# Kernel tuning notes

Measured on AMD Instinct MI355X. Metric: run time of the kernel, lower is better.

The kernel has to match this reference:

```python
import jax, jax.numpy as jnp
import numpy as np

P = 16
IMG_SIZES = [(512, 512), (512, 384), (448, 512), (384, 384), (320, 448), (256, 512), (384, 256), (512, 320)]
LMAX = 1024
B, DIM, HEADS, DH, DEPTH, MLP, NC = 8, 512, 8, 64, 6, 2048, 1000
PD = 3 * P * P  # 768 patch dim


def layer_norm(x, w, b=None, eps=1e-5):
    mu = x.mean(-1, keepdims=True)
    var = ((x - mu) ** 2).mean(-1, keepdims=True)
    y = (x - mu) * jax.lax.rsqrt(var + eps) * w
    return y + b if b is not None else y


def _pack(images):
    # slice each image to its true (static) resolution, patchify, pad to LMAX
    toks, his, wis, msks = [], [], [], []
    for i, (H, W) in enumerate(IMG_SIZES):
        h, w = H // P, W // P
        L = h * w
        img = images[i, :, :H, :W]
        t = img.reshape(3, h, P, w, P).transpose(1, 3, 0, 2, 4).reshape(L, PD)
        hi = jnp.repeat(jnp.arange(h), w)
        wi = jnp.tile(jnp.arange(w), h)
        pad = LMAX - L
        toks.append(jnp.pad(t, ((0, pad), (0, 0))))
        his.append(jnp.pad(hi, (0, pad)))
        wis.append(jnp.pad(wi, (0, pad)))
        msks.append(jnp.arange(LMAX) < L)
    return jnp.stack(toks), jnp.stack(his), jnp.stack(wis), jnp.stack(msks)


def _mha(qx, kx, kmask, wq, wk, wv, qn, kn, wo):
    Bq, Lq, _ = qx.shape
    Lk = kx.shape[1]
    q = (qx @ wq.T).reshape(Bq, Lq, HEADS, DH)
    k = (kx @ wk.T).reshape(Bq, Lk, HEADS, DH)
    v = (kx @ wv.T).reshape(Bq, Lk, HEADS, DH)
    q = layer_norm(q, qn)
    k = layer_norm(k, kn)
    s = jnp.einsum('bqhd,bkhd->bhqk', q, k) / np.sqrt(DH).astype(np.float32)
    s = s + jnp.where(kmask[:, None, None, :], 0.0, -1e9)
    a = jax.nn.softmax(s, axis=-1)
    o = jnp.einsum('bhqk,bkhd->bqhd', a, v).reshape(Bq, Lq, HEADS * DH)
    return o @ wo.T


def setup_inputs() -> dict:
    key = jax.random.key(0)
    ks = iter(jax.random.split(key, 48))

    def nrm(shape, s=0.02):
        return jax.random.normal(next(ks), shape, jnp.float32) * s

    return {
        'images': jax.random.normal(next(ks), (B, 3, 512, 512), jnp.float32),
        'pe_ln1_w': jnp.ones(PD), 'pe_ln1_b': jnp.zeros(PD),
        'pe_w': nrm((DIM, PD)), 'pe_b': jnp.zeros(DIM),
        'pe_ln2_w': jnp.ones(DIM), 'pe_ln2_b': jnp.zeros(DIM),
        'pos_h': nrm((32, DIM), 1.0), 'pos_w': nrm((32, DIM), 1.0),
        'attn_ln': jnp.ones((DEPTH, DIM)),
        'wq': nrm((DEPTH, DIM, DIM)), 'wk': nrm((DEPTH, DIM, DIM)), 'wv': nrm((DEPTH, DIM, DIM)),
        'qn': jnp.ones((DEPTH, DH)), 'kn': jnp.ones((DEPTH, DH)),
        'wo': nrm((DEPTH, DIM, DIM)),
        'ff_ln': jnp.ones((DEPTH, DIM)),
        'ff_w1': nrm((DEPTH, MLP, DIM)), 'ff_b1': jnp.zeros((DEPTH, MLP)),
        'ff_w2': nrm((DEPTH, DIM, MLP)), 'ff_b2': jnp.zeros((DEPTH, DIM)),
        'final_ln': jnp.ones(DIM),
        'pool_q': nrm((DIM,), 1.0), 'pool_ln': jnp.ones(DIM),
        'pool_wq': nrm((DIM, DIM)), 'pool_wk': nrm((DIM, DIM)), 'pool_wv': nrm((DIM, DIM)),
        'pool_qn': jnp.ones(DH), 'pool_kn': jnp.ones(DH),
        'pool_wo': nrm((DIM, DIM)),
        'head_ln': jnp.ones(DIM), 'head_w': nrm((NC, DIM)),
    }


def reference(images, pe_ln1_w, pe_ln1_b, pe_w, pe_b, pe_ln2_w, pe_ln2_b, pos_h, pos_w,
              attn_ln, wq, wk, wv, qn, kn, wo, ff_ln, ff_w1, ff_b1, ff_w2, ff_b2,
              final_ln, pool_q, pool_ln, pool_wq, pool_wk, pool_wv, pool_qn, pool_kn,
              pool_wo, head_ln, head_w):
    tok, hi, wi, mask = _pack(images)
    t = layer_norm(tok, pe_ln1_w, pe_ln1_b)
    t = t @ pe_w.T + pe_b
    t = layer_norm(t, pe_ln2_w, pe_ln2_b)
    t = t + pos_h[hi] + pos_w[wi]
    t = t * mask[..., None]
    for l in range(DEPTH):
        xn = layer_norm(t, attn_ln[l])
        t = t + _mha(xn, xn, mask, wq[l], wk[l], wv[l], qn[l], kn[l], wo[l])
        h = layer_norm(t, ff_ln[l])
        t = t + (jax.nn.gelu(h @ ff_w1[l].T + ff_b1[l], approximate=False) @ ff_w2[l].T + ff_b2[l])
    t = layer_norm(t, final_ln)
    # attention pooling: one learned query per image; context = transformer output (unnormed inside attn)
    q = jnp.broadcast_to(pool_q, (B, 1, DIM))
    qn_ = layer_norm(q, pool_ln)
    pooled = _mha(qn_, t, mask, pool_wq, pool_wk, pool_wv, pool_qn, pool_kn, pool_wo)[:, 0]
    return layer_norm(pooled, head_ln) @ head_w.T
```

## Files before the change

kernel.cpp:

```cpp
#include <hip/hip_runtime.h>
#include <math.h>

#define LMAXS 1024
#define NB 8
#define DIM 512
#define HEADS 8
#define DH 64
#define DEPTH 6
#define MLP 2048
#define NC 1000
#define PDIM 768
#define MPACK 5376
#define MVALID 5360

typedef __attribute__((ext_vector_type(8))) short short8;
typedef __attribute__((ext_vector_type(4))) float floatx4;
typedef unsigned short ushort;

__constant__ int c_w[8]   = {32,24,32,24,28,32,16,20};
__constant__ int c_L[8]   = {1024,768,896,576,560,512,384,640};
__constant__ int c_off[9] = {0,1024,1792,2688,3264,3824,4336,4720,5360};

__device__ __forceinline__ int row2img(int r) {
  int b = 0;
  #pragma unroll
  for (int i = 1; i < 8; ++i) if (r >= c_off[i]) b = i;
  return b;
}

__device__ __forceinline__ ushort f2bf(float x) {
  unsigned int u = __float_as_uint(x);
  u += 0x7fff + ((u >> 16) & 1);
  return (ushort)(u >> 16);
}

#define GLOAD_LDS16(gp, lp) \
  __builtin_amdgcn_global_load_lds((const __attribute__((address_space(1))) void*)(gp), \
                                   (__attribute__((address_space(3))) void*)(lp), 16, 0, 0)

__device__ __forceinline__ void reduce2_256(float& s, float& s2, float* red) {
  #pragma unroll
  for (int off = 32; off; off >>= 1) {
    s  += __shfl_xor(s, off);
    s2 += __shfl_xor(s2, off);
  }
  int wv = threadIdx.x >> 6;
  if ((threadIdx.x & 63) == 0) { red[wv*2] = s; red[wv*2+1] = s2; }
  __syncthreads();
  s  = red[0] + red[2] + red[4] + red[6];
  s2 = red[1] + red[3] + red[5] + red[7];
  __syncthreads();
}

__global__ __launch_bounds__(256) void cvt_k(const float* __restrict__ s, ushort* __restrict__ d, int n) {
  int i = blockIdx.x*256 + threadIdx.x;
  if (i < n) d[i] = f2bf(s[i]);
}
__global__ __launch_bounds__(256) void cvt_qkv_k(
    const float* __restrict__ wq, const float* __restrict__ wk, const float* __restrict__ wv,
    ushort* __restrict__ d) {
  int i = blockIdx.x*256 + threadIdx.x;
  if (i >= 6*1536*512) return;
  int l = i / (1536*512), r = (i / 512) % 1536, k = i & 511;
  const float* src = (r < 512) ? wq : (r < 1024) ? wk : wv;
  int rr = r & 511;
  d[i] = f2bf(src[(size_t)l*DIM*DIM + (size_t)rr*DIM + k]);
}
__global__ __launch_bounds__(256) void cvt_pool_k(
    const float* __restrict__ wk, const float* __restrict__ wv, ushort* __restrict__ d) {
  int i = blockIdx.x*256 + threadIdx.x;
  if (i >= 1024*512) return;
  int r = i >> 9, k = i & 511;
  d[i] = f2bf(r < 512 ? wk[(size_t)r*DIM + k] : wv[(size_t)(r-512)*DIM + k]);
}

__global__ __launch_bounds__(256) void pack_ln1_k(
    const float* __restrict__ images, const float* __restrict__ g,
    const float* __restrict__ bb, ushort* __restrict__ tok) {
  int r = blockIdx.x;
  ushort* out = tok + (size_t)r * PDIM;
  if (r >= MVALID) {
    for (int i = threadIdx.x; i < PDIM; i += 256) out[i] = 0;
    return;
  }
  int b = row2img(r), l = r - c_off[b];
  int wgrid = c_w[b];
  __shared__ float vals[PDIM];
  __shared__ float red[8];
  int hp = l / wgrid, wp = l % wgrid;
  const float* base = images + (size_t)b*3*512*512 + (size_t)hp*16*512 + wp*16;
  float s = 0.f, s2 = 0.f;
  for (int i = threadIdx.x; i < PDIM; i += 256) {
    int c = i >> 8, rr = (i >> 4) & 15, cc = i & 15;
    float v = base[(size_t)c*512*512 + rr*512 + cc];
    vals[i] = v; s += v; s2 += v*v;
  }
  reduce2_256(s, s2, red);
  float mu = s * (1.f/PDIM);
  float rs = rsqrtf(fmaxf(s2*(1.f/PDIM) - mu*mu, 0.f) + 1e-5f);
  for (int i = threadIdx.x; i < PDIM; i += 256)
    out[i] = f2bf((vals[i]-mu)*rs*g[i] + bb[i]);
}

template<int ACT, int OUT>
__global__ __launch_bounds__(256) void gemm_bf(
    const ushort* __restrict__ A, const ushort* __restrict__ W,
    const float* __restrict__ bias, void* __restrict__ Cv,
    int M, int N, int K) {
  __shared__ ushort As[128*64];
  __shared__ ushort Ws[128*64];
  int tid = threadIdx.x;
  int row0 = blockIdx.y*128, col0 = blockIdx.x*128;
  int lane = tid & 63, l15 = lane & 15, quad = lane >> 4;
  int wv = tid >> 6, wm = wv >> 1, wn = wv & 1;
  int sw = l15 & 7;
  int segA = (quad ^ sw) * 8, segB = segA ^ 32;
  const ushort *Ap[4], *Wp[4];
  #pragma unroll
  for (int j = 0; j < 4; ++j) {
    int blk = j*256 + tid;
    int r = blk >> 3, s = ((blk & 7) ^ (r & 7)) * 8;
    Ap[j] = A + (size_t)(row0 + r)*K + s;
    Wp[j] = W + (size_t)(col0 + r)*K + s;
  }
  int ksl = K / gridDim.z;
  int kb0 = blockIdx.z * ksl;
  floatx4 acc[4][4] = {};
  for (int k0 = kb0; k0 < kb0 + ksl; k0 += 64) {
    __syncthreads();
    #pragma unroll
    for (int j = 0; j < 4; ++j) {
      GLOAD_LDS16(Ap[j] + k0, &As[(j*256+tid)*8]);
      GLOAD_LDS16(Wp[j] + k0, &Ws[(j*256+tid)*8]);
    }
    __syncthreads();
    #pragma unroll
    for (int w = 0; w < 2; ++w) {
      int sg = w ? segB : segA;
      short8 af[4], bf[4];
      #pragma unroll
      for (int i = 0; i < 4; ++i) af[i] = *(const short8*)&As[(wm*64 + i*16 + l15)*64 + sg];
      #pragma unroll
      for (int j = 0; j < 4; ++j) bf[j] = *(const short8*)&Ws[(wn*64 + j*16 + l15)*64 + sg];
      #pragma unroll
      for (int i = 0; i < 4; ++i)
        #pragma unroll
        for (int j = 0; j < 4; ++j)
          acc[i][j] = __builtin_amdgcn_mfma_f32_16x16x32_bf16(af[i], bf[j], acc[i][j], 0, 0, 0);
    }
  }
  int rb = row0 + wm*64 + quad*4;
  int cb = col0 + wn*64 + l15;
  bool addb = (bias != nullptr) && (blockIdx.z == 0);
  #pragma unroll
  for (int j = 0; j < 4; ++j) {
    int cc = cb + j*16;
    float bsum = addb ? bias[cc] : 0.f;
    #pragma unroll
    for (int i = 0; i < 4; ++i) {
      int rr = rb + i*16;
      #pragma unroll
      for (int reg = 0; reg < 4; ++reg) {
        float v = acc[i][j][reg] + bsum;
        if (ACT == 1) v = 0.5f*v*(1.f + erff(v*0.70710678118654752f));
        size_t idx = (size_t)(rr + reg)*N + cc;
        if (OUT == 0)      ((float*)Cv)[idx] = v;
        else if (OUT == 1) unsafeAtomicAdd(&((float*)Cv)[idx], v);
        else               ((ushort*)Cv)[idx] = f2bf(v);
      }
    }
  }
}

template<int POOL>
__global__ __launch_bounds__(256) void gemm_qkv_k(
    const ushort* __restrict__ A, const ushort* __restrict__ W,
    const float* __restrict__ gq, const float* __restrict__ gk,
    ushort* __restrict__ Qh, ushort* __restrict__ Kh, ushort* __restrict__ Vh,
    float* __restrict__ KV, int N) {
  const int K = DIM;
  __shared__ ushort As[128*64];
  __shared__ ushort Ws[128*64];
  int tid = threadIdx.x;
  int row0 = blockIdx.y*128, col0 = blockIdx.x*128;
  int lane = tid & 63, l15 = lane & 15, quad = lane >> 4;
  int wv = tid >> 6, wm = wv >> 1, wn = wv & 1;
  int sw = l15 & 7;
  int segA = (quad ^ sw) * 8, segB = segA ^ 32;
  const ushort *Ap[4], *Wp[4];
  #pragma unroll
  for (int j = 0; j < 4; ++j) {
    int blk = j*256 + tid;
    int r = blk >> 3, s = ((blk & 7) ^ (r & 7)) * 8;
    Ap[j] = A + (size_t)(row0 + r)*K + s;
    Wp[j] = W + (size_t)(col0 + r)*K + s;
  }
  floatx4 acc[4][4] = {};
  for (int k0 = 0; k0 < K; k0 += 64) {
    __syncthreads();
    #pragma unroll
    for (int j = 0; j < 4; ++j) {
      GLOAD_LDS16(Ap[j] + k0, &As[(j*256+tid)*8]);
      GLOAD_LDS16(Wp[j] + k0, &Ws[(j*256+tid)*8]);
    }
    __syncthreads();
    #pragma unroll
    for (int w = 0; w < 2; ++w) {
      int sg = w ? segB : segA;
      short8 af[4], bf[4];
      #pragma unroll
      for (int i = 0; i < 4; ++i) af[i] = *(const short8*)&As[(wm*64 + i*16 + l15)*64 + sg];
      #pragma unroll
      for (int j = 0; j < 4; ++j) bf[j] = *(const short8*)&Ws[(wn*64 + j*16 + l15)*64 + sg];
      #pragma unroll
      for (int i = 0; i < 4; ++i)
        #pragma unroll
        for (int j = 0; j < 4; ++j)
          acc[i][j] = __builtin_amdgcn_mfma_f32_16x16x32_bf16(af[i], bf[j], acc[i][j], 0, 0, 0);
    }
  }
  int unit = (col0 >> 6) + wn;
  bool needln = POOL ? (unit < 8) : (unit < 16);
  const float* gain = POOL ? gq : (unit < 8 ? gq : gk);
  #pragma unroll
  for (int i = 0; i < 4; ++i) {
    float s[4] = {0,0,0,0}, s2[4] = {0,0,0,0};
    if (needln) {
      #pragma unroll
      for (int j = 0; j < 4; ++j)
        #pragma unroll
        for (int reg = 0; reg < 4; ++reg) {
          float v = acc[i][j][reg];
          s[reg] += v; s2[reg] += v*v;
        }
      #pragma unroll
      for (int reg = 0; reg < 4; ++reg)
        #pragma unroll
        for (int off = 1; off < 16; off <<= 1) {
          s[reg]  += __shfl_xor(s[reg],  off);
          s2[reg] += __shfl_xor(s2[reg], off);
        }
    }
    #pragma unroll
    for (int reg = 0; reg < 4; ++reg) {
      int r = row0 + wm*64 + i*16 + quad*4 + reg;
      if (r >= MVALID) continue;
      float mu = s[reg]*(1.f/64.f);
      float rs = rsqrtf(fmaxf(s2[reg]*(1.f/64.f) - mu*mu, 0.f) + 1e-5f);
      int b = row2img(r), l = r - c_off[b];
      #pragma unroll
      for (int j = 0; j < 4; ++j) {
        int dh = j*16 + l15;
        float v = acc[i][j][reg];
        if (needln) v = (v - mu)*rs*gain[dh];
        if (POOL) {
          KV[(size_t)r*1024 + unit*64 + dh] = v;
        } else {
          int h = unit & 7;
          size_t dst = ((size_t)(b*8+h)*LMAXS + l)*64 + dh;
          if (unit < 8)       Qh[dst] = f2bf(v);
          else if (unit < 16) Kh[dst] = f2bf(v);
          else                Vh[dst] = f2bf(v);
        }
      }
    }
  }
}

__global__ __launch_bounds__(256) void row_ln_bf_k(
    const float* __restrict__ X, const float* __restrict__ g,
    ushort* __restrict__ Y, int n) {
  __shared__ float red[8];
  size_t base = (size_t)blockIdx.x * n;
  float s=0.f, s2=0.f;
  for (int i = threadIdx.x; i < n; i += 256) { float v = X[base+i]; s += v; s2 += v*v; }
  reduce2_256(s, s2, red);
  float mu = s/n, rs = rsqrtf(fmaxf(s2/n - mu*mu, 0.f) + 1e-5f);
  for (int i = threadIdx.x; i < n; i += 256)
    Y[base+i] = f2bf((X[base+i]-mu)*rs*g[i]);
}

__global__ __launch_bounds__(256) void ln2_pos_k(
    float* __restrict__ T, const float* __restrict__ g, const float* __restrict__ bb,
    const float* __restrict__ ph, const float* __restrict__ pw) {
  int r = blockIdx.x;
  float* x = T + (size_t)r * DIM;
  if (r >= MVALID) {
    for (int i = threadIdx.x; i < DIM; i += 256) x[i] = 0.f;
    return;
  }
  int b = row2img(r), l = r - c_off[b];
  __shared__ float red[8];
  int wgrid = c_w[b];
  int hi = l / wgrid, wi = l % wgrid;
  float s=0.f, s2=0.f;
  for (int i = threadIdx.x; i < DIM; i += 256) { float v = x[i]; s+=v; s2+=v*v; }
  reduce2_256(s, s2, red);
  float mu = s*(1.f/DIM), rs = rsqrtf(fmaxf(s2*(1.f/DIM)-mu*mu, 0.f)+1e-5f);
  for (int i = threadIdx.x; i < DIM; i += 256)
    x[i] = (x[i]-mu)*rs*g[i] + bb[i] + ph[hi*DIM+i] + pw[wi*DIM+i];
}

__global__ __launch_bounds__(256) void vtrans_k(
    const ushort* __restrict__ Vh, ushort* __restrict__ VhT) {
  int bh = blockIdx.x, b = bh >> 3;
  int lt = blockIdx.y;
  if (lt*64 >= c_L[b]) return;
  __shared__ ushort t[64][72];
  int tid = threadIdx.x;
  int row = tid >> 2, seg = (tid & 3)*16;
  const ushort* src = Vh + ((size_t)bh*LMAXS + lt*64 + row)*64 + seg;
  *(short8*)&t[row][seg]   = *(const short8*)src;
  *(short8*)&t[row][seg+8] = *(const short8*)(src+8);
  __syncthreads();
  int dh = tid >> 2, ks = (tid & 3)*16;
  short8 o0, o1;
  #pragma unroll
  for (int jj = 0; jj < 8; ++jj) o0[jj] = (short)t[ks+jj][dh];
  #pragma unroll
  for (int jj = 0; jj < 8; ++jj) o1[jj] = (short)t[ks+8+jj][dh];
  ushort* dst = VhT + ((size_t)bh*64 + dh)*LMAXS + lt*64 + ks;
  *(short8*)dst     = o0;
  *(short8*)(dst+8) = o1;
}

__global__ __launch_bounds__(256) void attn_mfma_k(
    const ushort* __restrict__ Qh, const ushort* __restrict__ Kh,
    const ushort* __restrict__ VhT, ushort* __restrict__ O) {
  int bh = blockIdx.x, b = bh >> 3, h = bh & 7;
  int Lb = c_L[b];
  int qt = blockIdx.y;
  if (qt * 64 >= Lb) return;
  __shared__ ushort Ks[64*64];
  __shared__ ushort Vt[64*64];
  __shared__ ushort Pb[4][16][68];
  int tid = threadIdx.x, wv = tid >> 6, lane = tid & 63;
  int quad = lane >> 4, l15 = lane & 15;
  int sw = l15 & 7;
  int segA = (quad ^ sw) * 8, segB = segA ^ 32;
  int q0 = qt*64 + wv*16;
  bool active = q0 < Lb;
  const ushort* qhb = Qh + (size_t)bh * LMAXS * DH;
  const ushort* khb = Kh + (size_t)bh * LMAXS * DH;
  const ushort* vtb = VhT + (size_t)bh * DH * LMAXS;
  short8 aq0 = {}, aq1 = {};
  if (active) {
    const ushort* qp = qhb + (size_t)(q0 + l15) * DH;
    aq0 = *(const short8*)(qp + quad*8);
    aq1 = *(const short8*)(qp + 32 + quad*8);
  }
  int blk0 = tid, blk1 = tid + 256;
  int kr0 = blk0 >> 3, s0 = ((blk0 & 7) ^ (kr0 & 7)) * 8;
  int kr1 = blk1 >> 3, s1 = ((blk1 & 7) ^ (kr1 & 7)) * 8;
  const ushort* kg0 = khb + kr0*DH + s0;
  const ushort* kg1 = khb + kr1*DH + s1;
  const ushort* vg0 = vtb + (size_t)kr0*LMAXS + s0;
  const ushort* vg1 = vtb + (size_t)kr1*LMAXS + s1;
  float lsum[4] = {0.f,0.f,0.f,0.f};
  floatx4 o[4] = {};
  for (int kc = 0; kc < Lb; kc += 64) {
    __syncthreads();
    GLOAD_LDS16(kg0 + kc*DH, &Ks[blk0*8]);
    GLOAD_LDS16(kg1 + kc*DH, &Ks[blk1*8]);
    GLOAD_LDS16(vg0 + kc,    &Vt[blk0*8]);
    GLOAD_LDS16(vg1 + kc,    &Vt[blk1*8]);
    __syncthreads();
    if (!active) continue;
    bool tail = (kc + 64 > Lb);
    #pragma unroll
    for (int kb = 0; kb < 4; ++kb) {
      int krow = (kb*16 + l15) * 64;
      floatx4 s = {};
      s = __builtin_amdgcn_mfma_f32_16x16x32_bf16(aq0, *(const short8*)&Ks[krow + segA], s, 0,0,0);
      s = __builtin_amdgcn_mfma_f32_16x16x32_bf16(aq1, *(const short8*)&Ks[krow + segB], s, 0,0,0);
      #pragma unroll
      for (int reg = 0; reg < 4; ++reg) {
        float x = s[reg] * 0.125f;
        if (tail && (kc + kb*16 + l15 >= Lb)) x = -1e9f;
        float p = __expf(x);
        lsum[reg] += p;
        Pb[wv][quad*4+reg][kb*16+l15] = f2bf(p);
      }
    }
    short8 a0 = *(const short8*)&Pb[wv][l15][quad*8];
    short8 a1 = *(const short8*)&Pb[wv][l15][32+quad*8];
    #pragma unroll
    for (int nb = 0; nb < 4; ++nb) {
      int vrow = (nb*16 + l15) * 64;
      o[nb] = __builtin_amdgcn_mfma_f32_16x16x32_bf16(a0, *(const short8*)&Vt[vrow + segA], o[nb], 0,0,0);
      o[nb] = __builtin_amdgcn_mfma_f32_16x16x32_bf16(a1, *(const short8*)&Vt[vrow + segB], o[nb], 0,0,0);
    }
  }
  if (active) {
    float inv[4];
    #pragma unroll
    for (int reg = 0; reg < 4; ++reg) {
      float s = lsum[reg];
      s += __shfl_xor(s,1); s += __shfl_xor(s,2); s += __shfl_xor(s,4); s += __shfl_xor(s,8);
      inv[reg] = 1.f / s;
    }
    int rbase = c_off[b] + q0 + quad*4;
    #pragma unroll
    for (int nb = 0; nb < 4; ++nb)
      #pragma unroll
      for (int reg = 0; reg < 4; ++reg)
        O[(size_t)(rbase+reg)*DIM + h*DH + nb*16 + l15] = f2bf(o[nb][reg] * inv[reg]);
  }
}

__global__ __launch_bounds__(256) void pool_prep_a_k(
    const float* __restrict__ pq, const float* __restrict__ pln,
    const float* __restrict__ pwq, float* __restrict__ qp) {
  __shared__ float qln[DIM];
  __shared__ float red[8];
  int tid = threadIdx.x;
  float s=0.f, s2=0.f;
  for (int i=tid;i<DIM;i+=256){ float v=pq[i]; s+=v; s2+=v*v; }
  reduce2_256(s, s2, red);
  float mu=s*(1.f/DIM), rs=rsqrtf(fmaxf(s2*(1.f/DIM)-mu*mu,0.f)+1e-5f);
  for (int i=tid;i<DIM;i+=256) qln[i]=(pq[i]-mu)*rs*pln[i];
  __syncthreads();
  int n = blockIdx.x*64 + (tid>>2);
  int kq = (tid&3)*128;
  const float4* wr = (const float4*)(pwq + (size_t)n*DIM + kq);
  float a=0.f;
  #pragma unroll
  for (int k=0;k<32;++k) {
    float4 w4 = wr[k];
    float4 q4 = *(const float4*)&qln[kq + k*4];
    a += w4.x*q4.x + w4.y*q4.y + w4.z*q4.z + w4.w*q4.w;
  }
  a += __shfl_xor(a,1); a += __shfl_xor(a,2);
  if ((tid&3)==0) qp[n]=a;
}

__global__ __launch_bounds__(512) void pool_prep_b_k(
    const float* __restrict__ qp, const float* __restrict__ pqn, float* __restrict__ qpool) {
  int h = threadIdx.x >> 6, lane = threadIdx.x & 63;
  float v = qp[h*64 + lane];
  float s = v, s2 = v*v;
  #pragma unroll
  for (int off=32; off; off>>=1) { s += __shfl_xor(s,off); s2 += __shfl_xor(s2,off); }
  float mu = s*(1.f/64), rs = rsqrtf(fmaxf(s2*(1.f/64)-mu*mu, 0.f)+1e-5f);
  qpool[h*64+lane] = (v-mu)*rs*pqn[lane];
}

__global__ __launch_bounds__(256) void pool_attn_part_k(
    const float* __restrict__ qpool, const float* __restrict__ KV,
    float* __restrict__ PART) {
  __shared__ float qh[DH];
  __shared__ float ps[256];
  __shared__ float op[4][DH];
  __shared__ float red[8];
  int bh = blockIdx.x, c = blockIdx.y;
  int b = bh>>3, h = bh&7;
  int Lb = c_L[b];
  int tid = threadIdx.x;
  if (tid < DH) qh[tid] = qpool[h*DH + tid];
  __syncthreads();
  int kk = c*256 + tid;
  float p = 0.f;
  if (kk < Lb) {
    const float4* kp = (const float4*)(KV + (size_t)(c_off[b]+kk)*1024 + h*DH);
    float a = 0.f;
    #pragma unroll
    for (int dd=0; dd<16; ++dd) {
      float4 kv = kp[dd];
      a += kv.x*qh[dd*4] + kv.y*qh[dd*4+1] + kv.z*qh[dd*4+2] + kv.w*qh[dd*4+3];
    }
    p = __expf(a*0.125f);
  }
  ps[tid] = p;
  float s = p, s2 = 0.f;
  reduce2_256(s, s2, red);
  int wvv = tid >> 6, lane = tid & 63;
  float o = 0.f;
  int kb = c*256 + wvv*64;
  const float* vb = KV + (size_t)c_off[b]*1024 + 512 + h*DH + lane;
  for (int j = 0; j < 64; ++j) {
    int key = kb + j;
    if (key < Lb) o += ps[wvv*64+j] * vb[(size_t)key*1024];
  }
  op[wvv][lane] = o;
  __syncthreads();
  if (tid < DH)
    PART[((size_t)bh*4 + c)*66 + tid] = op[0][tid]+op[1][tid]+op[2][tid]+op[3][tid];
  if (tid == 64)
    PART[((size_t)bh*4 + c)*66 + 64] = s;
}

__global__ __launch_bounds__(64) void pool_attn_comb_k(
    const float* __restrict__ PART, float* __restrict__ O) {
  int bh = blockIdx.x, b = bh>>3, h = bh&7, d = threadIdx.x;
  float o = 0.f, sum = 0.f;
  #pragma unroll
  for (int c = 0; c < 4; ++c) {
    o   += PART[((size_t)bh*4 + c)*66 + d];
    sum += PART[((size_t)bh*4 + c)*66 + 64];
  }
  O[(size_t)b*DIM + h*DH + d] = o / sum;
}

__global__ __launch_bounds__(256) void proj512_k(
    const float* __restrict__ X, const float* __restrict__ W, float* __restrict__ Y) {
  __shared__ float xr[DIM];
  int b = blockIdx.x, tid = threadIdx.x;
  for (int i=tid;i<DIM;i+=256) xr[i] = X[(size_t)b*DIM+i];
  __syncthreads();
  if (tid < 128) {
    int n = blockIdx.y*128 + tid;
    const float4* wr = (const float4*)(W + (size_t)n*DIM);
    float a=0.f;
    for (int k=0;k<DIM/4;++k) { float4 w4 = wr[k]; a += w4.x*xr[k*4]+w4.y*xr[k*4+1]+w4.z*xr[k*4+2]+w4.w*xr[k*4+3]; }
    Y[(size_t)b*DIM+n]=a;
  }
}

__global__ __launch_bounds__(256) void head_out_k(
    const float* __restrict__ X, const float* __restrict__ g,
    const float* __restrict__ W, float* __restrict__ out) {
  __shared__ float xr[DIM];
  __shared__ float red[8];
  int b = blockIdx.x, tid = threadIdx.x;
  float s=0.f, s2=0.f;
  for (int i=tid;i<DIM;i+=256){ float v=X[(size_t)b*DIM+i]; s+=v; s2+=v*v; }
  reduce2_256(s, s2, red);
  float mu=s*(1.f/DIM), rs=rsqrtf(fmaxf(s2*(1.f/DIM)-mu*mu,0.f)+1e-5f);
  for (int i=tid;i<DIM;i+=256) xr[i]=(X[(size_t)b*DIM+i]-mu)*rs*g[i];
  __syncthreads();
  if (tid < 125) {
    int n = blockIdx.y*125 + tid;
    const float4* wr = (const float4*)(W + (size_t)n*DIM);
    float a=0.f;
    for (int k=0;k<DIM/4;++k){ float4 w4=wr[k]; a += w4.x*xr[k*4]+w4.y*xr[k*4+1]+w4.z*xr[k*4+2]+w4.w*xr[k*4+3]; }
    out[(size_t)b*NC+n]=a;
  }
}

extern "C" void kernel_launch(void* const* d_in, const int* in_sizes, int n_in,
                              void* d_out, int out_size, void* d_ws, size_t ws_size,
                              hipStream_t stream) {
  const float* images  = (const float*)d_in[0];
  const float* pe_ln1_w= (const float*)d_in[1];
  const float* pe_ln1_b= (const float*)d_in[2];
  const float* pe_w    = (const float*)d_in[3];
  const float* pe_b    = (const float*)d_in[4];
  const float* pe_ln2_w= (const float*)d_in[5];
  const float* pe_ln2_b= (const float*)d_in[6];
  const float* pos_h   = (const float*)d_in[7];
  const float* pos_w   = (const float*)d_in[8];
  const float* attn_ln = (const float*)d_in[9];
  const float* wq      = (const float*)d_in[10];
  const float* wk      = (const float*)d_in[11];
  const float* wvp     = (const float*)d_in[12];
  const float* qn      = (const float*)d_in[13];
  const float* kn      = (const float*)d_in[14];
  const float* wo      = (const float*)d_in[15];
  const float* ff_ln   = (const float*)d_in[16];
  const float* ff_w1   = (const float*)d_in[17];
  const float* ff_b1   = (const float*)d_in[18];
  const float* ff_w2   = (const float*)d_in[19];
  const float* ff_b2   = (const float*)d_in[20];
  const float* final_ln= (const float*)d_in[21];
  const float* pool_q  = (const float*)d_in[22];
  const float* pool_ln = (const float*)d_in[23];
  const float* pool_wq = (const float*)d_in[24];
  const float* pool_wk = (const float*)d_in[25];
  const float* pool_wv = (const float*)d_in[26];
  const float* pool_qn = (const float*)d_in[27];
  const float* pool_kn = (const float*)d_in[28];
  const float* pool_wo = (const float*)d_in[29];
  const float* head_ln = (const float*)d_in[30];
  const float* head_w  = (const float*)d_in[31];
  (void)ws_size; (void)in_sizes; (void)n_in; (void)out_size;

  char* p = (char*)d_ws;
  ushort* WQKVc = (ushort*)p; p += (size_t)6*1536*512*2;
  ushort* WOc   = (ushort*)p; p += (size_t)6*512*512*2;
  ushort* W1c   = (ushort*)p; p += (size_t)6*2048*512*2;
  ushort* W2c   = (ushort*)p; p += (size_t)6*512*2048*2;
  ushort* PEWc  = (ushort*)p; p += (size_t)512*768*2;
  ushort* PKVc  = (ushort*)p; p += (size_t)1024*512*2;
  float*  T     = (float*)p;  p += (size_t)MPACK*DIM*4;
  ushort* XN    = (ushort*)p; p += (size_t)MPACK*DIM*2;
  float*  KVb   = (float*)p;  p += (size_t)MPACK*1024*4;
  ushort* Qh    = (ushort*)p; p += (size_t)64*LMAXS*DH*2;
  ushort* Kh    = (ushort*)p; p += (size_t)64*LMAXS*DH*2;
  ushort* Vh    = (ushort*)p; p += (size_t)64*LMAXS*DH*2;
  ushort* VhT   = (ushort*)p; p += (size_t)64*64*LMAXS*2;
  ushort* FFH   = (ushort*)p; p += (size_t)MPACK*MLP*2;
  ushort* TOK   = FFH;
  ushort* ATTO  = FFH;
  float*  QP    = (float*)p;  p += DIM*4;
  float*  QPOOL = (float*)p;  p += DIM*4;
  float*  POOLO = (float*)p;  p += NB*DIM*4;
  float*  POOLED= (float*)p;  p += NB*DIM*4;
  float*  PART  = (float*)p;  p += (size_t)64*4*66*4;

  cvt_qkv_k<<<(6*1536*512+255)/256, 256, 0, stream>>>(wq, wk, wvp, WQKVc);
  cvt_k<<<(6*512*512+255)/256, 256, 0, stream>>>(wo, WOc, 6*512*512);
  cvt_k<<<(6*2048*512+255)/256, 256, 0, stream>>>(ff_w1, W1c, 6*2048*512);
  cvt_k<<<(6*512*2048+255)/256, 256, 0, stream>>>(ff_w2, W2c, 6*512*2048);
  cvt_k<<<(512*768+255)/256, 256, 0, stream>>>(pe_w, PEWc, 512*768);
  cvt_pool_k<<<(1024*512+255)/256, 256, 0, stream>>>(pool_wk, pool_wv, PKVc);

  pack_ln1_k<<<MPACK, 256, 0, stream>>>(images, pe_ln1_w, pe_ln1_b, TOK);
  gemm_bf<0,0><<<dim3(4, MPACK/128), 256, 0, stream>>>(TOK, PEWc, pe_b, T, MPACK, DIM, PDIM);
  ln2_pos_k<<<MPACK, 256, 0, stream>>>(T, pe_ln2_w, pe_ln2_b, pos_h, pos_w);

  for (int l = 0; l < DEPTH; ++l) {
    row_ln_bf_k<<<MPACK, 256, 0, stream>>>(T, attn_ln + l*DIM, XN, DIM);
    gemm_qkv_k<0><<<dim3(12, MPACK/128), 256, 0, stream>>>(
        XN, WQKVc + (size_t)l*1536*512, qn + l*DH, kn + l*DH, Qh, Kh, Vh, nullptr, 1536);
    vtrans_k<<<dim3(64, 16), 256, 0, stream>>>(Vh, VhT);
    attn_mfma_k<<<dim3(64, 16), 256, 0, stream>>>(Qh, Kh, VhT, ATTO);
    gemm_bf<0,1><<<dim3(4, MPACK/128, 2), 256, 0, stream>>>(ATTO, WOc + (size_t)l*512*512, nullptr, T, MPACK, DIM, DIM);
    row_ln_bf_k<<<MPACK, 256, 0, stream>>>(T, ff_ln + l*DIM, XN, DIM);
    gemm_bf<1,2><<<dim3(16, MPACK/128), 256, 0, stream>>>(XN, W1c + (size_t)l*MLP*DIM, ff_b1 + l*MLP, FFH, MPACK, MLP, DIM);
    gemm_bf<0,1><<<dim3(4, MPACK/128, 4), 256, 0, stream>>>(FFH, W2c + (size_t)l*DIM*MLP, ff_b2 + l*DIM, T, MPACK, DIM, MLP);
  }

  row_ln_bf_k<<<MPACK, 256, 0, stream>>>(T, final_ln, XN, DIM);
  pool_prep_a_k<<<8, 256, 0, stream>>>(pool_q, pool_ln, pool_wq, QP);
  pool_prep_b_k<<<1, 512, 0, stream>>>(QP, pool_qn, QPOOL);
  gemm_qkv_k<1><<<dim3(8, MPACK/128), 256, 0, stream>>>(
      XN, PKVc, pool_kn, nullptr, nullptr, nullptr, nullptr, KVb, 1024);
  pool_attn_part_k<<<dim3(64, 4), 256, 0, stream>>>(QPOOL, KVb, PART);
  pool_attn_comb_k<<<64, 64, 0, stream>>>(PART, POOLO);
  proj512_k<<<dim3(8, 4), 256, 0, stream>>>(POOLO, pool_wo, POOLED);
  head_out_k<<<dim3(8, 8), 256, 0, stream>>>(POOLED, head_ln, head_w, (float*)d_out);
}
```

Before: 1.445 ms.

## Replace split-K atomic accumulation with partial buffers reduced in fused LayerNorm

The split-K GEMMs for the attention output and FFN down projections now write their per-slice partials to two scratch buffers instead of doing atomic adds into the residual stream. The following LayerNorm kernel adds both partials into the residual, writes it back, and normalizes in the same pass, with the row length fixed at 512 values per row. The FFN down projection drops from four K-splits to two, which halves its grid parallelism. The change removes atomic traffic and makes the summation order deterministic, at the cost of extra partial-buffer writes and reads that reuse the pooling KV scratch area.

```diff
diff --git a/kernel.cpp b/kernel.cpp
--- a/kernel.cpp
+++ b/kernel.cpp
@@ -152,6 +152,7 @@
   int rb = row0 + wm*64 + quad*4;
   int cb = col0 + wn*64 + l15;
   bool addb = (bias != nullptr) && (blockIdx.z == 0);
+  float* outz = (float*)Cv + (OUT == 3 ? (size_t)blockIdx.z * M * N : 0);
   #pragma unroll
   for (int j = 0; j < 4; ++j) {
     int cc = cb + j*16;
@@ -165,7 +166,8 @@
         if (ACT == 1) v = 0.5f*v*(1.f + erff(v*0.70710678118654752f));
         size_t idx = (size_t)(rr + reg)*N + cc;
         if (OUT == 0)      ((float*)Cv)[idx] = v;
-        else if (OUT == 1) unsafeAtomicAdd(&((float*)Cv)[idx], v);
+        else if (OUT == 1) ((float*)Cv)[idx] += v;
+        else if (OUT == 3) outz[idx] = v;
         else               ((ushort*)Cv)[idx] = f2bf(v);
       }
     }
@@ -267,17 +269,23 @@
   }
 }
 
-__global__ __launch_bounds__(256) void row_ln_bf_k(
-    const float* __restrict__ X, const float* __restrict__ g,
-    ushort* __restrict__ Y, int n) {
+__global__ __launch_bounds__(256) void row_ln_add2_k(
+    float* __restrict__ T, const float* __restrict__ P0, const float* __restrict__ P1,
+    const float* __restrict__ g, ushort* __restrict__ Y) {
   __shared__ float red[8];
-  size_t base = (size_t)blockIdx.x * n;
-  float s=0.f, s2=0.f;
-  for (int i = threadIdx.x; i < n; i += 256) { float v = X[base+i]; s += v; s2 += v*v; }
+  size_t base = (size_t)blockIdx.x * DIM;
+  float v0 = T[base + threadIdx.x], v1 = T[base + threadIdx.x + 256];
+  if (P0) {
+    v0 += P0[base + threadIdx.x] + P1[base + threadIdx.x];
+    v1 += P0[base + threadIdx.x + 256] + P1[base + threadIdx.x + 256];
+    T[base + threadIdx.x] = v0;
+    T[base + threadIdx.x + 256] = v1;
+  }
+  float s = v0 + v1, s2 = v0*v0 + v1*v1;
   reduce2_256(s, s2, red);
-  float mu = s/n, rs = rsqrtf(fmaxf(s2/n - mu*mu, 0.f) + 1e-5f);
-  for (int i = threadIdx.x; i < n; i += 256)
-    Y[base+i] = f2bf((X[base+i]-mu)*rs*g[i]);
+  float mu = s*(1.f/DIM), rs = rsqrtf(fmaxf(s2*(1.f/DIM) - mu*mu, 0.f) + 1e-5f);
+  Y[base + threadIdx.x]       = f2bf((v0-mu)*rs*g[threadIdx.x]);
+  Y[base + threadIdx.x + 256] = f2bf((v1-mu)*rs*g[threadIdx.x + 256]);
 }
 
 __global__ __launch_bounds__(256) void ln2_pos_k(
@@ -584,6 +592,8 @@
   float*  T     = (float*)p;  p += (size_t)MPACK*DIM*4;
   ushort* XN    = (ushort*)p; p += (size_t)MPACK*DIM*2;
   float*  KVb   = (float*)p;  p += (size_t)MPACK*1024*4;
+  float*  P0    = KVb;
+  float*  P1    = KVb + (size_t)MPACK*DIM;
   ushort* Qh    = (ushort*)p; p += (size_t)64*LMAXS*DH*2;
   ushort* Kh    = (ushort*)p; p += (size_t)64*LMAXS*DH*2;
   ushort* Vh    = (ushort*)p; p += (size_t)64*LMAXS*DH*2;
@@ -609,18 +619,18 @@
   ln2_pos_k<<<MPACK, 256, 0, stream>>>(T, pe_ln2_w, pe_ln2_b, pos_h, pos_w);
 
   for (int l = 0; l < DEPTH; ++l) {
-    row_ln_bf_k<<<MPACK, 256, 0, stream>>>(T, attn_ln + l*DIM, XN, DIM);
+    row_ln_add2_k<<<MPACK, 256, 0, stream>>>(T, l ? P0 : nullptr, P1, attn_ln + l*DIM, XN);
     gemm_qkv_k<0><<<dim3(12, MPACK/128), 256, 0, stream>>>(
         XN, WQKVc + (size_t)l*1536*512, qn + l*DH, kn + l*DH, Qh, Kh, Vh, nullptr, 1536);
     vtrans_k<<<dim3(64, 16), 256, 0, stream>>>(Vh, VhT);
     attn_mfma_k<<<dim3(64, 16), 256, 0, stream>>>(Qh, Kh, VhT, ATTO);
-    gemm_bf<0,1><<<dim3(4, MPACK/128, 2), 256, 0, stream>>>(ATTO, WOc + (size_t)l*512*512, nullptr, T, MPACK, DIM, DIM);
-    row_ln_bf_k<<<MPACK, 256, 0, stream>>>(T, ff_ln + l*DIM, XN, DIM);
+    gemm_bf<0,3><<<dim3(4, MPACK/128, 2), 256, 0, stream>>>(ATTO, WOc + (size_t)l*512*512, nullptr, P0, MPACK, DIM, DIM);
+    row_ln_add2_k<<<MPACK, 256, 0, stream>>>(T, P0, P1, ff_ln + l*DIM, XN);
     gemm_bf<1,2><<<dim3(16, MPACK/128), 256, 0, stream>>>(XN, W1c + (size_t)l*MLP*DIM, ff_b1 + l*MLP, FFH, MPACK, MLP, DIM);
-    gemm_bf<0,1><<<dim3(4, MPACK/128, 4), 256, 0, stream>>>(FFH, W2c + (size_t)l*DIM*MLP, ff_b2 + l*DIM, T, MPACK, DIM, MLP);
-  }
-
-  row_ln_bf_k<<<MPACK, 256, 0, stream>>>(T, final_ln, XN, DIM);
+    gemm_bf<0,3><<<dim3(4, MPACK/128, 2), 256, 0, stream>>>(FFH, W2c + (size_t)l*DIM*MLP, ff_b2 + l*DIM, P0, MPACK, DIM, MLP);
+  }
+
+  row_ln_add2_k<<<MPACK, 256, 0, stream>>>(T, P0, P1, final_ln, XN);
   pool_prep_a_k<<<8, 256, 0, stream>>>(pool_q, pool_ln, pool_wq, QP);
   pool_prep_b_k<<<1, 512, 0, stream>>>(QP, pool_qn, QPOOL);
   gemm_qkv_k<1><<<dim3(8, MPACK/128), 256, 0, stream>>>(
```

Result: faster. 1.265 ms (-12.5%).
